# Performance work log

Hardware: AMD Instinct MI355X
Metric: run time of the kernel (lower is better)

The kernel has to match this reference:

```python
import jax, jax.numpy as jnp
import numpy as np


def setup_inputs() -> dict:
    key = jax.random.key(0)
    k1, k2 = jax.random.split(key)
    B, T, D = 32, 2048, 64
    NUM_CODES = 1024
    z_e = jax.random.normal(k1, (B, T, D), dtype=jnp.float32)
    codebook = jax.random.normal(k2, (NUM_CODES, D), dtype=jnp.float32)
    return {"z_e": z_e, "codebook": codebook}


def reference(z_e, codebook):
    # z_e: [B, T, D], codebook: [K, D]
    B, T, D = z_e.shape
    z_flat = z_e.reshape(-1, D)  # [N, D], N = B*T
    x2 = jnp.sum(z_flat * z_flat, axis=-1, keepdims=True)          # [N, 1]
    c2 = jnp.sum(codebook * codebook, axis=-1)                      # [K]
    xc = jnp.einsum('nd,kd->nk', z_flat, codebook)                  # [N, K]
    dists = x2 - 2.0 * xc + c2[None, :]                              # [N, K]
    indices = jnp.argmin(dists, axis=1)                              # [N]
    z_q = codebook[indices].reshape(B, T, D)
    # Straight-through estimator
    z_q_st = z_e + jax.lax.stop_gradient(z_q - z_e)
    return z_q_st, indices.reshape(B, T)
```

## Files before the change

kernel.cpp:

```cpp
#include <hip/hip_runtime.h>


typedef __attribute__((ext_vector_type(8))) short short8;
typedef __attribute__((ext_vector_type(4))) float f32x4;

#define N_ROWS  65536
#define D       64
#define K_CODES 1024
#define DELTA_H 1.5f
#define CAP     16

__device__ __forceinline__ unsigned short f2bf(float f) {
    unsigned u = __builtin_bit_cast(unsigned, f);
    unsigned r = (u + 0x7fffu + ((u >> 16) & 1u)) >> 16;
    return (unsigned short)r;
}

__device__ __forceinline__ short8 cvt8(float4 u, float4 v) {
    short8 r;
    r[0] = (short)f2bf(u.x); r[1] = (short)f2bf(u.y);
    r[2] = (short)f2bf(u.z); r[3] = (short)f2bf(u.w);
    r[4] = (short)f2bf(v.x); r[5] = (short)f2bf(v.y);
    r[6] = (short)f2bf(v.z); r[7] = (short)f2bf(v.w);
    return r;
}

__device__ __forceinline__ float dist_f32(const float* __restrict__ xr,
                                          const float* __restrict__ cr,
                                          float c2k) {
    float a = 0.f, b = 0.f, c = 0.f, d = 0.f;
#pragma unroll
    for (int i = 0; i < 16; i += 2) {
        const float4 x0 = ((const float4*)xr)[i];
        const float4 c0 = ((const float4*)cr)[i];
        const float4 x1 = ((const float4*)xr)[i + 1];
        const float4 c1 = ((const float4*)cr)[i + 1];
        a = fmaf(x0.x, c0.x, a); b = fmaf(x0.y, c0.y, b);
        c = fmaf(x0.z, c0.z, c); d = fmaf(x0.w, c0.w, d);
        a = fmaf(x1.x, c1.x, a); b = fmaf(x1.y, c1.y, b);
        c = fmaf(x1.z, c1.z, c); d = fmaf(x1.w, c1.w, d);
    }
    const float dot = (a + b) + (c + d);
    return fmaf(-2.f, dot, c2k);
}

__global__ __launch_bounds__(256) void prep_kernel(const float* __restrict__ cb,
                                                   float* __restrict__ c2,
                                                   unsigned short* __restrict__ cbb) {
    const int c = blockIdx.x * 256 + threadIdx.x;
    const float4* row = (const float4*)(cb + (size_t)c * D);
    unsigned short* orow = cbb + (size_t)c * D;
    float s0 = 0.f, s1 = 0.f, s2 = 0.f, s3 = 0.f;
#pragma unroll
    for (int i = 0; i < 16; ++i) {
        const float4 v = row[i];
        s0 = fmaf(v.x, v.x, s0);
        s1 = fmaf(v.y, v.y, s1);
        s2 = fmaf(v.z, v.z, s2);
        s3 = fmaf(v.w, v.w, s3);
        ushort4 o;
        o.x = f2bf(v.x); o.y = f2bf(v.y); o.z = f2bf(v.z); o.w = f2bf(v.w);
        *(ushort4*)(orow + 4 * i) = o;
    }
    c2[c] = (s0 + s1) + (s2 + s3);
}

__global__ __launch_bounds__(256, 2) void vq_kernel(const float* __restrict__ z_e,
                                                    const float* __restrict__ cb,
                                                    const float* __restrict__ c2g,
                                                    const unsigned short* __restrict__ cbb,
                                                    float* __restrict__ out) {
    __shared__ int cnt_s[128];
    __shared__ int ovf_s[128];
    __shared__ int win_s[128];
    __shared__ int cand_s[128][CAP];

    const int tid   = threadIdx.x;
    const int w     = tid >> 6;
    const int lane  = tid & 63;
    const int lcol  = lane & 15;
    const int lk    = lane >> 4;
    const int rbase = blockIdx.x * 128 + w * 32;

    if (tid < 128) { cnt_s[tid] = 0; ovf_s[tid] = 0; }

    short8 a00, a01, a10, a11;
    {
        const float* p0 = z_e + (size_t)(rbase + lcol) * D + 8 * lk;
        const float* p1 = z_e + (size_t)(rbase + 16 + lcol) * D + 8 * lk;
        float4 u, v;
        u = *(const float4*)(p0);      v = *(const float4*)(p0 + 4);  a00 = cvt8(u, v);
        u = *(const float4*)(p0 + 32); v = *(const float4*)(p0 + 36); a01 = cvt8(u, v);
        u = *(const float4*)(p1);      v = *(const float4*)(p1 + 4);  a10 = cvt8(u, v);
        u = *(const float4*)(p1 + 32); v = *(const float4*)(p1 + 36); a11 = cvt8(u, v);
    }
    __syncthreads();

    const unsigned short* bp = cbb + (size_t)lcol * D + 8 * lk;

#define TILE_LOADS(T)                                                        \
    bn0 = *(const short8*)(bp + (size_t)(T) * 1024);                         \
    bn1 = *(const short8*)(bp + (size_t)(T) * 1024 + 32);                    \
    c2n = c2g[(T) * 16 + lcol];

#define TILE_MFMA()                                                          \
    const float sv = -0.5f * c2c;                                            \
    f32x4 acc0 = {sv, sv, sv, sv};                                           \
    f32x4 acc1 = {sv, sv, sv, sv};                                           \
    acc0 = __builtin_amdgcn_mfma_f32_16x16x32_bf16(a00, bc0, acc0, 0, 0, 0); \
    acc0 = __builtin_amdgcn_mfma_f32_16x16x32_bf16(a01, bc1, acc0, 0, 0, 0); \
    acc1 = __builtin_amdgcn_mfma_f32_16x16x32_bf16(a10, bc0, acc1, 0, 0, 0); \
    acc1 = __builtin_amdgcn_mfma_f32_16x16x32_bf16(a11, bc1, acc1, 0, 0, 0);

    float m00 = -3.4e38f, m01 = -3.4e38f, m02 = -3.4e38f, m03 = -3.4e38f;
    float m10 = -3.4e38f, m11 = -3.4e38f, m12 = -3.4e38f, m13 = -3.4e38f;
    {
        short8 bc0, bc1, bn0, bn1;
        float c2c, c2n;
        TILE_LOADS(0);
        bc0 = bn0; bc1 = bn1; c2c = c2n;
        for (int t = 0; t < 64; ++t) {
            if (t < 63) { TILE_LOADS(t + 1); }
            TILE_MFMA();
            m00 = fmaxf(m00, acc0[0]); m01 = fmaxf(m01, acc0[1]);
            m02 = fmaxf(m02, acc0[2]); m03 = fmaxf(m03, acc0[3]);
            m10 = fmaxf(m10, acc1[0]); m11 = fmaxf(m11, acc1[1]);
            m12 = fmaxf(m12, acc1[2]); m13 = fmaxf(m13, acc1[3]);
            bc0 = bn0; bc1 = bn1; c2c = c2n;
        }
    }

#pragma unroll
    for (int off = 1; off < 16; off <<= 1) {
        m00 = fmaxf(m00, __shfl_xor(m00, off));
        m01 = fmaxf(m01, __shfl_xor(m01, off));
        m02 = fmaxf(m02, __shfl_xor(m02, off));
        m03 = fmaxf(m03, __shfl_xor(m03, off));
        m10 = fmaxf(m10, __shfl_xor(m10, off));
        m11 = fmaxf(m11, __shfl_xor(m11, off));
        m12 = fmaxf(m12, __shfl_xor(m12, off));
        m13 = fmaxf(m13, __shfl_xor(m13, off));
    }
    const float g0 = fminf(fminf(m00, m01), fminf(m02, m03)) - DELTA_H;
    const float g1 = fminf(fminf(m10, m11), fminf(m12, m13)) - DELTA_H;

#define REC(RL, CODE)                                                        \
    {                                                                        \
        const int sl = atomicAdd(&cnt_s[RL], 1);                             \
        if (sl < CAP) cand_s[RL][sl] = (CODE); else ovf_s[RL] = 1;           \
    }

    {
        short8 bc0, bc1, bn0, bn1;
        float c2c, c2n;
        TILE_LOADS(0);
        bc0 = bn0; bc1 = bn1; c2c = c2n;
        for (int t = 0; t < 64; ++t) {
            if (t < 63) { TILE_LOADS(t + 1); }
            TILE_MFMA();
            const float t0 = fmaxf(fmaxf(acc0[0], acc0[1]), fmaxf(acc0[2], acc0[3]));
            const float t1 = fmaxf(fmaxf(acc1[0], acc1[1]), fmaxf(acc1[2], acc1[3]));
            if (t0 >= g0) {
                const int code = t * 16 + lcol;
                const int rl = w * 32 + 4 * lk;
                if (acc0[0] >= m00 - DELTA_H) REC(rl + 0, code);
                if (acc0[1] >= m01 - DELTA_H) REC(rl + 1, code);
                if (acc0[2] >= m02 - DELTA_H) REC(rl + 2, code);
                if (acc0[3] >= m03 - DELTA_H) REC(rl + 3, code);
            }
            if (t1 >= g1) {
                const int code = t * 16 + lcol;
                const int rl = w * 32 + 16 + 4 * lk;
                if (acc1[0] >= m10 - DELTA_H) REC(rl + 0, code);
                if (acc1[1] >= m11 - DELTA_H) REC(rl + 1, code);
                if (acc1[2] >= m12 - DELTA_H) REC(rl + 2, code);
                if (acc1[3] >= m13 - DELTA_H) REC(rl + 3, code);
            }
            bc0 = bn0; bc1 = bn1; c2c = c2n;
        }
    }
    __syncthreads();

    if (tid < 128) {
        const int grow = blockIdx.x * 128 + tid;
        const int cnt  = cnt_s[tid];
        int win;
        if (ovf_s[tid] == 0 && cnt == 1) {
            win = cand_s[tid][0];
        } else {
            const float* xr = z_e + (size_t)grow * D;
            float bestd = 3.4e38f;
            int   bi    = K_CODES;
            if (ovf_s[tid]) {
                for (int k = 0; k < K_CODES; ++k) {
                    const float dk = dist_f32(xr, cb + (size_t)k * D, c2g[k]);
                    if (dk < bestd || (dk == bestd && k < bi)) { bestd = dk; bi = k; }
                }
            } else {
                for (int j = 0; j < cnt; ++j) {
                    const int k = cand_s[tid][j];
                    const float dk = dist_f32(xr, cb + (size_t)k * D, c2g[k]);
                    if (dk < bestd || (dk == bestd && k < bi)) { bestd = dk; bi = k; }
                }
            }
            win = bi;
        }
        win_s[tid] = win;
        out[(size_t)N_ROWS * D + grow] = (float)win;
    }
    __syncthreads();

    {
        const int rl   = tid >> 1;
        const int hf   = tid & 1;
        const int grow = blockIdx.x * 128 + rl;
        const float4* src = (const float4*)(cb + (size_t)win_s[rl] * D) + hf * 8;
        float4*       dst = (float4*)(out + (size_t)grow * D) + hf * 8;
#pragma unroll
        for (int i = 0; i < 8; ++i) dst[i] = src[i];
    }
}

extern "C" void kernel_launch(void* const* d_in, const int* in_sizes, int n_in,
                              void* d_out, int out_size, void* d_ws, size_t ws_size,
                              hipStream_t stream) {
    const float* z_e = (const float*)d_in[0];
    const float* cb  = (const float*)d_in[1];
    float* out = (float*)d_out;
    float*          c2  = (float*)d_ws;
    unsigned short* cbb = (unsigned short*)((char*)d_ws + 4096);

    hipLaunchKernelGGL(prep_kernel, dim3(K_CODES / 256), dim3(256), 0, stream,
                       cb, c2, cbb);
    hipLaunchKernelGGL(vq_kernel, dim3(N_ROWS / 128), dim3(256), 0, stream,
                       z_e, cb, c2, cbb, out);
}
```

Baseline: 147.7 us.

## Halve rows per wave, raise occupancy, double-buffer codebook tiles

```diff
diff --git a/kernel.cpp b/kernel.cpp
--- a/kernel.cpp
+++ b/kernel.cpp
@@ -47,142 +47,150 @@
 __global__ __launch_bounds__(256) void prep_kernel(const float* __restrict__ cb,
                                                    float* __restrict__ c2,
                                                    unsigned short* __restrict__ cbb) {
-    const int c = blockIdx.x * 256 + threadIdx.x;
-    const float4* row = (const float4*)(cb + (size_t)c * D);
-    unsigned short* orow = cbb + (size_t)c * D;
-    float s0 = 0.f, s1 = 0.f, s2 = 0.f, s3 = 0.f;
-#pragma unroll
-    for (int i = 0; i < 16; ++i) {
-        const float4 v = row[i];
-        s0 = fmaf(v.x, v.x, s0);
-        s1 = fmaf(v.y, v.y, s1);
-        s2 = fmaf(v.z, v.z, s2);
-        s3 = fmaf(v.w, v.w, s3);
-        ushort4 o;
-        o.x = f2bf(v.x); o.y = f2bf(v.y); o.z = f2bf(v.z); o.w = f2bf(v.w);
-        *(ushort4*)(orow + 4 * i) = o;
-    }
-    c2[c] = (s0 + s1) + (s2 + s3);
-}
-
-__global__ __launch_bounds__(256, 2) void vq_kernel(const float* __restrict__ z_e,
+    const int gt = blockIdx.x * 256 + threadIdx.x;
+    const int c  = gt >> 1;
+    const int h  = gt & 1;
+    const float* src = cb + (size_t)c * D + h * 32;
+    unsigned short* dst = cbb + (size_t)c * D + h * 32;
+    float s = 0.f;
+#pragma unroll
+    for (int i = 0; i < 4; ++i) {
+        const float4 u = ((const float4*)src)[2 * i];
+        const float4 v = ((const float4*)src)[2 * i + 1];
+        s = fmaf(u.x, u.x, s); s = fmaf(u.y, u.y, s);
+        s = fmaf(u.z, u.z, s); s = fmaf(u.w, u.w, s);
+        s = fmaf(v.x, v.x, s); s = fmaf(v.y, v.y, s);
+        s = fmaf(v.z, v.z, s); s = fmaf(v.w, v.w, s);
+        *(short8*)(dst + 8 * i) = cvt8(u, v);
+    }
+    const float o = __shfl_xor(s, 1);
+    if (h == 0) c2[c] = s + o;
+}
+
+__global__ __launch_bounds__(256, 4) void vq_kernel(const float* __restrict__ z_e,
                                                     const float* __restrict__ cb,
                                                     const float* __restrict__ c2g,
                                                     const unsigned short* __restrict__ cbb,
                                                     float* __restrict__ out) {
-    __shared__ int cnt_s[128];
-    __shared__ int ovf_s[128];
-    __shared__ int win_s[128];
-    __shared__ int cand_s[128][CAP];
+    __shared__ int cnt_s[64];
+    __shared__ int ovf_s[64];
+    __shared__ int win_s[64];
+    __shared__ int cand_s[64][CAP];
 
     const int tid   = threadIdx.x;
     const int w     = tid >> 6;
     const int lane  = tid & 63;
     const int lcol  = lane & 15;
     const int lk    = lane >> 4;
-    const int rbase = blockIdx.x * 128 + w * 32;
-
-    if (tid < 128) { cnt_s[tid] = 0; ovf_s[tid] = 0; }
-
-    short8 a00, a01, a10, a11;
-    {
-        const float* p0 = z_e + (size_t)(rbase + lcol) * D + 8 * lk;
-        const float* p1 = z_e + (size_t)(rbase + 16 + lcol) * D + 8 * lk;
-        float4 u, v;
-        u = *(const float4*)(p0);      v = *(const float4*)(p0 + 4);  a00 = cvt8(u, v);
-        u = *(const float4*)(p0 + 32); v = *(const float4*)(p0 + 36); a01 = cvt8(u, v);
-        u = *(const float4*)(p1);      v = *(const float4*)(p1 + 4);  a10 = cvt8(u, v);
-        u = *(const float4*)(p1 + 32); v = *(const float4*)(p1 + 36); a11 = cvt8(u, v);
+    const int rbase = blockIdx.x * 64 + w * 16;
+
+    if (tid < 64) { cnt_s[tid] = 0; ovf_s[tid] = 0; }
+
+    short8 a0, a1;
+    {
+        const float* p = z_e + (size_t)(rbase + lcol) * D + 8 * lk;
+        a0 = cvt8(*(const float4*)p,        *(const float4*)(p + 4));
+        a1 = cvt8(*(const float4*)(p + 32), *(const float4*)(p + 36));
     }
     __syncthreads();
 
-    const unsigned short* bp = cbb + (size_t)lcol * D + 8 * lk;
-
-#define TILE_LOADS(T)                                                        \
-    bn0 = *(const short8*)(bp + (size_t)(T) * 1024);                         \
-    bn1 = *(const short8*)(bp + (size_t)(T) * 1024 + 32);                    \
-    c2n = c2g[(T) * 16 + lcol];
-
-#define TILE_MFMA()                                                          \
-    const float sv = -0.5f * c2c;                                            \
-    f32x4 acc0 = {sv, sv, sv, sv};                                           \
-    f32x4 acc1 = {sv, sv, sv, sv};                                           \
-    acc0 = __builtin_amdgcn_mfma_f32_16x16x32_bf16(a00, bc0, acc0, 0, 0, 0); \
-    acc0 = __builtin_amdgcn_mfma_f32_16x16x32_bf16(a01, bc1, acc0, 0, 0, 0); \
-    acc1 = __builtin_amdgcn_mfma_f32_16x16x32_bf16(a10, bc0, acc1, 0, 0, 0); \
-    acc1 = __builtin_amdgcn_mfma_f32_16x16x32_bf16(a11, bc1, acc1, 0, 0, 0);
-
-    float m00 = -3.4e38f, m01 = -3.4e38f, m02 = -3.4e38f, m03 = -3.4e38f;
-    float m10 = -3.4e38f, m11 = -3.4e38f, m12 = -3.4e38f, m13 = -3.4e38f;
-    {
-        short8 bc0, bc1, bn0, bn1;
-        float c2c, c2n;
-        TILE_LOADS(0);
-        bc0 = bn0; bc1 = bn1; c2c = c2n;
-        for (int t = 0; t < 64; ++t) {
-            if (t < 63) { TILE_LOADS(t + 1); }
-            TILE_MFMA();
-            m00 = fmaxf(m00, acc0[0]); m01 = fmaxf(m01, acc0[1]);
-            m02 = fmaxf(m02, acc0[2]); m03 = fmaxf(m03, acc0[3]);
-            m10 = fmaxf(m10, acc1[0]); m11 = fmaxf(m11, acc1[1]);
-            m12 = fmaxf(m12, acc1[2]); m13 = fmaxf(m13, acc1[3]);
-            bc0 = bn0; bc1 = bn1; c2c = c2n;
+    const unsigned short* bp  = cbb + (size_t)lcol * D + 8 * lk;
+    const float*          c2p = c2g + lcol;
+
+#define LOADSET(S, T)                                                 \
+    b0##S = *(const short8*)(bp + (size_t)(T) * 1024);                \
+    b1##S = *(const short8*)(bp + (size_t)(T) * 1024 + 32);           \
+    c2##S = c2p[(T) * 16];
+
+#define MFMASET(S)                                                            \
+    f32x4 acc##S = {0.f, 0.f, 0.f, 0.f};                                      \
+    acc##S = __builtin_amdgcn_mfma_f32_16x16x32_bf16(a0, b0##S, acc##S, 0,0,0); \
+    acc##S = __builtin_amdgcn_mfma_f32_16x16x32_bf16(a1, b1##S, acc##S, 0,0,0);
+
+    float m0 = -3.4e38f, m1 = -3.4e38f, m2 = -3.4e38f, m3 = -3.4e38f;
+    {
+        short8 b0A, b1A, b0B, b1B;
+        float c2A, c2B;
+        LOADSET(A, 0); LOADSET(B, 1);
+        for (int t = 0; t < 64; t += 2) {
+            {
+                MFMASET(A);
+                const float cA = c2A;
+                LOADSET(A, (t + 2) & 63);
+                m0 = fmaxf(m0, fmaf(-0.5f, cA, accA[0]));
+                m1 = fmaxf(m1, fmaf(-0.5f, cA, accA[1]));
+                m2 = fmaxf(m2, fmaf(-0.5f, cA, accA[2]));
+                m3 = fmaxf(m3, fmaf(-0.5f, cA, accA[3]));
+            }
+            {
+                MFMASET(B);
+                const float cB = c2B;
+                LOADSET(B, (t + 3) & 63);
+                m0 = fmaxf(m0, fmaf(-0.5f, cB, accB[0]));
+                m1 = fmaxf(m1, fmaf(-0.5f, cB, accB[1]));
+                m2 = fmaxf(m2, fmaf(-0.5f, cB, accB[2]));
+                m3 = fmaxf(m3, fmaf(-0.5f, cB, accB[3]));
+            }
         }
     }
 
 #pragma unroll
     for (int off = 1; off < 16; off <<= 1) {
-        m00 = fmaxf(m00, __shfl_xor(m00, off));
-        m01 = fmaxf(m01, __shfl_xor(m01, off));
-        m02 = fmaxf(m02, __shfl_xor(m02, off));
-        m03 = fmaxf(m03, __shfl_xor(m03, off));
-        m10 = fmaxf(m10, __shfl_xor(m10, off));
-        m11 = fmaxf(m11, __shfl_xor(m11, off));
-        m12 = fmaxf(m12, __shfl_xor(m12, off));
-        m13 = fmaxf(m13, __shfl_xor(m13, off));
-    }
-    const float g0 = fminf(fminf(m00, m01), fminf(m02, m03)) - DELTA_H;
-    const float g1 = fminf(fminf(m10, m11), fminf(m12, m13)) - DELTA_H;
-
-#define REC(RL, CODE)                                                        \
-    {                                                                        \
-        const int sl = atomicAdd(&cnt_s[RL], 1);                             \
-        if (sl < CAP) cand_s[RL][sl] = (CODE); else ovf_s[RL] = 1;           \
-    }
-
-    {
-        short8 bc0, bc1, bn0, bn1;
-        float c2c, c2n;
-        TILE_LOADS(0);
-        bc0 = bn0; bc1 = bn1; c2c = c2n;
-        for (int t = 0; t < 64; ++t) {
-            if (t < 63) { TILE_LOADS(t + 1); }
-            TILE_MFMA();
-            const float t0 = fmaxf(fmaxf(acc0[0], acc0[1]), fmaxf(acc0[2], acc0[3]));
-            const float t1 = fmaxf(fmaxf(acc1[0], acc1[1]), fmaxf(acc1[2], acc1[3]));
-            if (t0 >= g0) {
-                const int code = t * 16 + lcol;
-                const int rl = w * 32 + 4 * lk;
-                if (acc0[0] >= m00 - DELTA_H) REC(rl + 0, code);
-                if (acc0[1] >= m01 - DELTA_H) REC(rl + 1, code);
-                if (acc0[2] >= m02 - DELTA_H) REC(rl + 2, code);
-                if (acc0[3] >= m03 - DELTA_H) REC(rl + 3, code);
-            }
-            if (t1 >= g1) {
-                const int code = t * 16 + lcol;
-                const int rl = w * 32 + 16 + 4 * lk;
-                if (acc1[0] >= m10 - DELTA_H) REC(rl + 0, code);
-                if (acc1[1] >= m11 - DELTA_H) REC(rl + 1, code);
-                if (acc1[2] >= m12 - DELTA_H) REC(rl + 2, code);
-                if (acc1[3] >= m13 - DELTA_H) REC(rl + 3, code);
-            }
-            bc0 = bn0; bc1 = bn1; c2c = c2n;
+        m0 = fmaxf(m0, __shfl_xor(m0, off));
+        m1 = fmaxf(m1, __shfl_xor(m1, off));
+        m2 = fmaxf(m2, __shfl_xor(m2, off));
+        m3 = fmaxf(m3, __shfl_xor(m3, off));
+    }
+    const float gmin = fminf(fminf(m0, m1), fminf(m2, m3)) - DELTA_H;
+    const float h0 = m0 - DELTA_H, h1 = m1 - DELTA_H;
+    const float h2 = m2 - DELTA_H, h3 = m3 - DELTA_H;
+
+#define REC(RL, CODE)                                                 \
+    {                                                                 \
+        const int sl = atomicAdd(&cnt_s[RL], 1);                      \
+        if (sl < CAP) cand_s[RL][sl] = (CODE); else ovf_s[RL] = 1;    \
+    }
+
+#define SWEEP2(S, TT)                                                 \
+    {                                                                 \
+        const float t0 = fmaf(-0.5f, c##S, acc##S[0]);                \
+        const float t1 = fmaf(-0.5f, c##S, acc##S[1]);                \
+        const float t2 = fmaf(-0.5f, c##S, acc##S[2]);                \
+        const float t3 = fmaf(-0.5f, c##S, acc##S[3]);                \
+        const float tm = fmaxf(fmaxf(t0, t1), fmaxf(t2, t3));         \
+        if (tm >= gmin) {                                             \
+            const int code = (TT) * 16 + lcol;                        \
+            const int rl   = w * 16 + 4 * lk;                         \
+            if (t0 >= h0) REC(rl + 0, code);                          \
+            if (t1 >= h1) REC(rl + 1, code);                          \
+            if (t2 >= h2) REC(rl + 2, code);                          \
+            if (t3 >= h3) REC(rl + 3, code);                          \
+        }                                                             \
+    }
+
+    {
+        short8 b0A, b1A, b0B, b1B;
+        float c2A, c2B;
+        LOADSET(A, 0); LOADSET(B, 1);
+        for (int t = 0; t < 64; t += 2) {
+            {
+                MFMASET(A);
+                const float cA = c2A;
+                LOADSET(A, (t + 2) & 63);
+                SWEEP2(A, t);
+            }
+            {
+                MFMASET(B);
+                const float cB = c2B;
+                LOADSET(B, (t + 3) & 63);
+                SWEEP2(B, t + 1);
+            }
         }
     }
     __syncthreads();
 
-    if (tid < 128) {
-        const int grow = blockIdx.x * 128 + tid;
+    if (tid < 64) {
+        const int grow = blockIdx.x * 64 + tid;
         const int cnt  = cnt_s[tid];
         int win;
         if (ovf_s[tid] == 0 && cnt == 1) {
@@ -211,13 +219,13 @@
     __syncthreads();
 
     {
-        const int rl   = tid >> 1;
-        const int hf   = tid & 1;
-        const int grow = blockIdx.x * 128 + rl;
-        const float4* src = (const float4*)(cb + (size_t)win_s[rl] * D) + hf * 8;
-        float4*       dst = (float4*)(out + (size_t)grow * D) + hf * 8;
-#pragma unroll
-        for (int i = 0; i < 8; ++i) dst[i] = src[i];
+        const int rl   = tid >> 2;
+        const int q    = tid & 3;
+        const int grow = blockIdx.x * 64 + rl;
+        const float4* src = (const float4*)(cb + (size_t)win_s[rl] * D) + q * 4;
+        float4*       dst = (float4*)(out + (size_t)grow * D) + q * 4;
+#pragma unroll
+        for (int i = 0; i < 4; ++i) dst[i] = src[i];
     }
 }
 
@@ -230,8 +238,7 @@
     float*          c2  = (float*)d_ws;
     unsigned short* cbb = (unsigned short*)((char*)d_ws + 4096);
 
-    hipLaunchKernelGGL(prep_kernel, dim3(K_CODES / 256), dim3(256), 0, stream,
-                       cb, c2, cbb);
-    hipLaunchKernelGGL(vq_kernel, dim3(N_ROWS / 128), dim3(256), 0, stream,
+    hipLaunchKernelGGL(prep_kernel, dim3(8), dim3(256), 0, stream, cb, c2, cbb);
+    hipLaunchKernelGGL(vq_kernel, dim3(N_ROWS / 64), dim3(256), 0, stream,
                        z_e, cb, c2, cbb, out);
 }
```

Measured after the change: 202.1 us. 1.37x slower.

## Split codebook across waves, each wave covering all 128 rows of the block

Applied to the files above, without the earlier changes.

```diff
diff --git a/kernel.cpp b/kernel.cpp
--- a/kernel.cpp
+++ b/kernel.cpp
@@ -9,6 +9,8 @@
 #define K_CODES 1024
 #define DELTA_H 1.5f
 #define CAP     16
+
+#define TILES(F) F(0) F(1) F(2) F(3) F(4) F(5) F(6) F(7)
 
 __device__ __forceinline__ unsigned short f2bf(float f) {
     unsigned u = __builtin_bit_cast(unsigned, f);
@@ -47,22 +49,25 @@
 __global__ __launch_bounds__(256) void prep_kernel(const float* __restrict__ cb,
                                                    float* __restrict__ c2,
                                                    unsigned short* __restrict__ cbb) {
-    const int c = blockIdx.x * 256 + threadIdx.x;
-    const float4* row = (const float4*)(cb + (size_t)c * D);
-    unsigned short* orow = cbb + (size_t)c * D;
-    float s0 = 0.f, s1 = 0.f, s2 = 0.f, s3 = 0.f;
+    const int gt = blockIdx.x * 256 + threadIdx.x;
+    const int c  = gt >> 2;
+    const int q  = gt & 3;
+    const float* src = cb + (size_t)c * D + q * 16;
+    unsigned short* dst = cbb + (size_t)c * D + q * 16;
+    float s = 0.f;
 #pragma unroll
-    for (int i = 0; i < 16; ++i) {
-        const float4 v = row[i];
-        s0 = fmaf(v.x, v.x, s0);
-        s1 = fmaf(v.y, v.y, s1);
-        s2 = fmaf(v.z, v.z, s2);
-        s3 = fmaf(v.w, v.w, s3);
-        ushort4 o;
-        o.x = f2bf(v.x); o.y = f2bf(v.y); o.z = f2bf(v.z); o.w = f2bf(v.w);
-        *(ushort4*)(orow + 4 * i) = o;
-    }
-    c2[c] = (s0 + s1) + (s2 + s3);
+    for (int i = 0; i < 2; ++i) {
+        const float4 u = ((const float4*)src)[2 * i];
+        const float4 v = ((const float4*)src)[2 * i + 1];
+        s = fmaf(u.x, u.x, s); s = fmaf(u.y, u.y, s);
+        s = fmaf(u.z, u.z, s); s = fmaf(u.w, u.w, s);
+        s = fmaf(v.x, v.x, s); s = fmaf(v.y, v.y, s);
+        s = fmaf(v.z, v.z, s); s = fmaf(v.w, v.w, s);
+        *(short8*)(dst + 8 * i) = cvt8(u, v);
+    }
+    s += __shfl_xor(s, 1);
+    s += __shfl_xor(s, 2);
+    if (q == 0) c2[c] = s;
 }
 
 __global__ __launch_bounds__(256, 2) void vq_kernel(const float* __restrict__ z_e,
@@ -70,119 +75,163 @@
                                                     const float* __restrict__ c2g,
                                                     const unsigned short* __restrict__ cbb,
                                                     float* __restrict__ out) {
-    __shared__ int cnt_s[128];
-    __shared__ int ovf_s[128];
-    __shared__ int win_s[128];
-    __shared__ int cand_s[128][CAP];
+    __shared__ float qmax_s[4][128];
+    __shared__ float gmax_s[128];
+    __shared__ int   cnt_s[128];
+    __shared__ int   ovf_s[128];
+    __shared__ int   win_s[128];
+    __shared__ int   cand_s[128][CAP];
 
     const int tid   = threadIdx.x;
     const int w     = tid >> 6;
     const int lane  = tid & 63;
     const int lcol  = lane & 15;
     const int lk    = lane >> 4;
-    const int rbase = blockIdx.x * 128 + w * 32;
+    const int rbase = blockIdx.x * 128;
 
     if (tid < 128) { cnt_s[tid] = 0; ovf_s[tid] = 0; }
 
-    short8 a00, a01, a10, a11;
-    {
-        const float* p0 = z_e + (size_t)(rbase + lcol) * D + 8 * lk;
-        const float* p1 = z_e + (size_t)(rbase + 16 + lcol) * D + 8 * lk;
-        float4 u, v;
-        u = *(const float4*)(p0);      v = *(const float4*)(p0 + 4);  a00 = cvt8(u, v);
-        u = *(const float4*)(p0 + 32); v = *(const float4*)(p0 + 36); a01 = cvt8(u, v);
-        u = *(const float4*)(p1);      v = *(const float4*)(p1 + 4);  a10 = cvt8(u, v);
-        u = *(const float4*)(p1 + 32); v = *(const float4*)(p1 + 36); a11 = cvt8(u, v);
-    }
-    __syncthreads();
-
-    const unsigned short* bp = cbb + (size_t)lcol * D + 8 * lk;
-
-#define TILE_LOADS(T)                                                        \
-    bn0 = *(const short8*)(bp + (size_t)(T) * 1024);                         \
-    bn1 = *(const short8*)(bp + (size_t)(T) * 1024 + 32);                    \
-    c2n = c2g[(T) * 16 + lcol];
-
-#define TILE_MFMA()                                                          \
-    const float sv = -0.5f * c2c;                                            \
-    f32x4 acc0 = {sv, sv, sv, sv};                                           \
-    f32x4 acc1 = {sv, sv, sv, sv};                                           \
-    acc0 = __builtin_amdgcn_mfma_f32_16x16x32_bf16(a00, bc0, acc0, 0, 0, 0); \
-    acc0 = __builtin_amdgcn_mfma_f32_16x16x32_bf16(a01, bc1, acc0, 0, 0, 0); \
-    acc1 = __builtin_amdgcn_mfma_f32_16x16x32_bf16(a10, bc0, acc1, 0, 0, 0); \
-    acc1 = __builtin_amdgcn_mfma_f32_16x16x32_bf16(a11, bc1, acc1, 0, 0, 0);
-
-    float m00 = -3.4e38f, m01 = -3.4e38f, m02 = -3.4e38f, m03 = -3.4e38f;
-    float m10 = -3.4e38f, m11 = -3.4e38f, m12 = -3.4e38f, m13 = -3.4e38f;
+#define DECLA(i) short8 a0_##i, a1_##i;
+    TILES(DECLA)
+#define LOADA(i)                                                               \
+    {                                                                          \
+        const float* p = z_e + (size_t)(rbase + 16 * (i) + lcol) * D + 8 * lk; \
+        a0_##i = cvt8(*(const float4*)p,        *(const float4*)(p + 4));      \
+        a1_##i = cvt8(*(const float4*)(p + 32), *(const float4*)(p + 36));     \
+    }
+    TILES(LOADA)
+
+    const unsigned short* bp  = cbb + (size_t)(w * 256 + lcol) * D + 8 * lk;
+    const float*          c2p = c2g + w * 256 + lcol;
+
+#define LOADB(T)                                                      \
+    bn0 = *(const short8*)(bp + (size_t)(T) * 1024);                  \
+    bn1 = *(const short8*)(bp + (size_t)(T) * 1024 + 32);             \
+    c2n = c2p[(T) * 16];
+
+#define MFMA16()                                                               \
+    const float sv = -0.5f * c2c;                                              \
+    _Pragma("unroll")                                                          \
+    TILES(DOMFMA)
+
+#define DOMFMA(i)                                                              \
+    f32x4 acc##i = {sv, sv, sv, sv};                                           \
+    acc##i = __builtin_amdgcn_mfma_f32_16x16x32_bf16(a0_##i, bc0, acc##i, 0, 0, 0); \
+    acc##i = __builtin_amdgcn_mfma_f32_16x16x32_bf16(a1_##i, bc1, acc##i, 0, 0, 0);
+
+#define DECLM(i) float m##i##0 = -3.4e38f, m##i##1 = -3.4e38f,                 \
+                       m##i##2 = -3.4e38f, m##i##3 = -3.4e38f;
+    TILES(DECLM)
     {
         short8 bc0, bc1, bn0, bn1;
         float c2c, c2n;
-        TILE_LOADS(0);
+        LOADB(0);
         bc0 = bn0; bc1 = bn1; c2c = c2n;
-        for (int t = 0; t < 64; ++t) {
-            if (t < 63) { TILE_LOADS(t + 1); }
-            TILE_MFMA();
-            m00 = fmaxf(m00, acc0[0]); m01 = fmaxf(m01, acc0[1]);
-            m02 = fmaxf(m02, acc0[2]); m03 = fmaxf(m03, acc0[3]);
-            m10 = fmaxf(m10, acc1[0]); m11 = fmaxf(m11, acc1[1]);
-            m12 = fmaxf(m12, acc1[2]); m13 = fmaxf(m13, acc1[3]);
-            bc0 = bn0; bc1 = bn1; c2c = c2n;
-        }
-    }
-
-#pragma unroll
-    for (int off = 1; off < 16; off <<= 1) {
-        m00 = fmaxf(m00, __shfl_xor(m00, off));
-        m01 = fmaxf(m01, __shfl_xor(m01, off));
-        m02 = fmaxf(m02, __shfl_xor(m02, off));
-        m03 = fmaxf(m03, __shfl_xor(m03, off));
-        m10 = fmaxf(m10, __shfl_xor(m10, off));
-        m11 = fmaxf(m11, __shfl_xor(m11, off));
-        m12 = fmaxf(m12, __shfl_xor(m12, off));
-        m13 = fmaxf(m13, __shfl_xor(m13, off));
-    }
-    const float g0 = fminf(fminf(m00, m01), fminf(m02, m03)) - DELTA_H;
-    const float g1 = fminf(fminf(m10, m11), fminf(m12, m13)) - DELTA_H;
-
-#define REC(RL, CODE)                                                        \
-    {                                                                        \
-        const int sl = atomicAdd(&cnt_s[RL], 1);                             \
-        if (sl < CAP) cand_s[RL][sl] = (CODE); else ovf_s[RL] = 1;           \
-    }
-
-    {
-        short8 bc0, bc1, bn0, bn1;
-        float c2c, c2n;
-        TILE_LOADS(0);
-        bc0 = bn0; bc1 = bn1; c2c = c2n;
-        for (int t = 0; t < 64; ++t) {
-            if (t < 63) { TILE_LOADS(t + 1); }
-            TILE_MFMA();
-            const float t0 = fmaxf(fmaxf(acc0[0], acc0[1]), fmaxf(acc0[2], acc0[3]));
-            const float t1 = fmaxf(fmaxf(acc1[0], acc1[1]), fmaxf(acc1[2], acc1[3]));
-            if (t0 >= g0) {
-                const int code = t * 16 + lcol;
-                const int rl = w * 32 + 4 * lk;
-                if (acc0[0] >= m00 - DELTA_H) REC(rl + 0, code);
-                if (acc0[1] >= m01 - DELTA_H) REC(rl + 1, code);
-                if (acc0[2] >= m02 - DELTA_H) REC(rl + 2, code);
-                if (acc0[3] >= m03 - DELTA_H) REC(rl + 3, code);
-            }
-            if (t1 >= g1) {
-                const int code = t * 16 + lcol;
-                const int rl = w * 32 + 16 + 4 * lk;
-                if (acc1[0] >= m10 - DELTA_H) REC(rl + 0, code);
-                if (acc1[1] >= m11 - DELTA_H) REC(rl + 1, code);
-                if (acc1[2] >= m12 - DELTA_H) REC(rl + 2, code);
-                if (acc1[3] >= m13 - DELTA_H) REC(rl + 3, code);
+        for (int tt = 0; tt < 16; ++tt) {
+            if (tt < 15) { LOADB(tt + 1); }
+            {
+                const float sv = -0.5f * c2c;
+#define DOTILE1(i)                                                                    \
+                f32x4 acc##i = {sv, sv, sv, sv};                                      \
+                acc##i = __builtin_amdgcn_mfma_f32_16x16x32_bf16(a0_##i, bc0, acc##i, 0, 0, 0); \
+                acc##i = __builtin_amdgcn_mfma_f32_16x16x32_bf16(a1_##i, bc1, acc##i, 0, 0, 0); \
+                m##i##0 = fmaxf(m##i##0, acc##i[0]);                                  \
+                m##i##1 = fmaxf(m##i##1, acc##i[1]);                                  \
+                m##i##2 = fmaxf(m##i##2, acc##i[2]);                                  \
+                m##i##3 = fmaxf(m##i##3, acc##i[3]);
+                TILES(DOTILE1)
             }
             bc0 = bn0; bc1 = bn1; c2c = c2n;
         }
     }
-    __syncthreads();
-
+
+#define REDT(i)                                                       \
+    m##i##0 = fmaxf(m##i##0, __shfl_xor(m##i##0, OFF));               \
+    m##i##1 = fmaxf(m##i##1, __shfl_xor(m##i##1, OFF));               \
+    m##i##2 = fmaxf(m##i##2, __shfl_xor(m##i##2, OFF));               \
+    m##i##3 = fmaxf(m##i##3, __shfl_xor(m##i##3, OFF));
+    {
+#define OFF 1
+        TILES(REDT)
+#undef OFF
+#define OFF 2
+        TILES(REDT)
+#undef OFF
+#define OFF 4
+        TILES(REDT)
+#undef OFF
+#define OFF 8
+        TILES(REDT)
+#undef OFF
+    }
+
+    if (lcol == 0) {
+#define WRQ(i)                                                        \
+        qmax_s[w][16 * (i) + 4 * lk + 0] = m##i##0;                   \
+        qmax_s[w][16 * (i) + 4 * lk + 1] = m##i##1;                   \
+        qmax_s[w][16 * (i) + 4 * lk + 2] = m##i##2;                   \
+        qmax_s[w][16 * (i) + 4 * lk + 3] = m##i##3;
+        TILES(WRQ)
+    }
+    __syncthreads();
     if (tid < 128) {
-        const int grow = blockIdx.x * 128 + tid;
+        gmax_s[tid] = fmaxf(fmaxf(qmax_s[0][tid], qmax_s[1][tid]),
+                            fmaxf(qmax_s[2][tid], qmax_s[3][tid]));
+    }
+    __syncthreads();
+
+#define DECLH(i)                                                      \
+    const float h##i##0 = gmax_s[16 * (i) + 4 * lk + 0] - DELTA_H;    \
+    const float h##i##1 = gmax_s[16 * (i) + 4 * lk + 1] - DELTA_H;    \
+    const float h##i##2 = gmax_s[16 * (i) + 4 * lk + 2] - DELTA_H;    \
+    const float h##i##3 = gmax_s[16 * (i) + 4 * lk + 3] - DELTA_H;
+    TILES(DECLH)
+#define MIN4(i) fminf(fminf(h##i##0, h##i##1), fminf(h##i##2, h##i##3))
+    const float gmin = fminf(
+        fminf(fminf(MIN4(0), MIN4(1)), fminf(MIN4(2), MIN4(3))),
+        fminf(fminf(MIN4(4), MIN4(5)), fminf(MIN4(6), MIN4(7))));
+
+#define REC(RL, CODE)                                                 \
+    {                                                                 \
+        const int sl = atomicAdd(&cnt_s[RL], 1);                      \
+        if (sl < CAP) cand_s[RL][sl] = (CODE); else ovf_s[RL] = 1;    \
+    }
+
+    {
+        short8 bc0, bc1, bn0, bn1;
+        float c2c, c2n;
+        LOADB(0);
+        bc0 = bn0; bc1 = bn1; c2c = c2n;
+        for (int tt = 0; tt < 16; ++tt) {
+            if (tt < 15) { LOADB(tt + 1); }
+            {
+                const float sv = -0.5f * c2c;
+#define DOTILE2(i)                                                                    \
+                f32x4 acc##i = {sv, sv, sv, sv};                                      \
+                acc##i = __builtin_amdgcn_mfma_f32_16x16x32_bf16(a0_##i, bc0, acc##i, 0, 0, 0); \
+                acc##i = __builtin_amdgcn_mfma_f32_16x16x32_bf16(a1_##i, bc1, acc##i, 0, 0, 0);
+                TILES(DOTILE2)
+#define MAX4(i) fmaxf(fmaxf(acc##i[0], acc##i[1]), fmaxf(acc##i[2], acc##i[3]))
+                const float tm = fmaxf(
+                    fmaxf(fmaxf(MAX4(0), MAX4(1)), fmaxf(MAX4(2), MAX4(3))),
+                    fmaxf(fmaxf(MAX4(4), MAX4(5)), fmaxf(MAX4(6), MAX4(7))));
+                if (tm >= gmin) {
+                    const int code = (w << 8) + (tt << 4) + lcol;
+#define CHK(i)                                                            \
+                    if (acc##i[0] >= h##i##0) REC(16 * (i) + 4 * lk + 0, code); \
+                    if (acc##i[1] >= h##i##1) REC(16 * (i) + 4 * lk + 1, code); \
+                    if (acc##i[2] >= h##i##2) REC(16 * (i) + 4 * lk + 2, code); \
+                    if (acc##i[3] >= h##i##3) REC(16 * (i) + 4 * lk + 3, code);
+                    TILES(CHK)
+                }
+            }
+            bc0 = bn0; bc1 = bn1; c2c = c2n;
+        }
+    }
+    __syncthreads();
+
+    if (tid < 128) {
+        const int grow = rbase + tid;
         const int cnt  = cnt_s[tid];
         int win;
         if (ovf_s[tid] == 0 && cnt == 1) {
@@ -213,7 +262,7 @@
     {
         const int rl   = tid >> 1;
         const int hf   = tid & 1;
-        const int grow = blockIdx.x * 128 + rl;
+        const int grow = rbase + rl;
         const float4* src = (const float4*)(cb + (size_t)win_s[rl] * D) + hf * 8;
         float4*       dst = (float4*)(out + (size_t)grow * D) + hf * 8;
 #pragma unroll
@@ -230,8 +279,7 @@
     float*          c2  = (float*)d_ws;
     unsigned short* cbb = (unsigned short*)((char*)d_ws + 4096);
 
-    hipLaunchKernelGGL(prep_kernel, dim3(K_CODES / 256), dim3(256), 0, stream,
-                       cb, c2, cbb);
+    hipLaunchKernelGGL(prep_kernel, dim3(16), dim3(256), 0, stream, cb, c2, cbb);
     hipLaunchKernelGGL(vq_kernel, dim3(N_ROWS / 128), dim3(256), 0, stream,
                        z_e, cb, c2, cbb, out);
 }
```

Measured after the change: 119.0 us. -19.4%, faster.
